# Optimization experiments

Measured on AMD Instinct MI355X. Metric: run time of the kernel, lower is better.

## Reference

```python
import jax, jax.numpy as jnp
import numpy as np

N_NODES = 50000
N_EDGES = 800000
NODE_F = 256
EDGE_F = 8
OUT_F = 64
NEG_SLOPE = 0.2
EPS = 1e-9


def _xavier(key, shape):
    # xavier_normal_ with gain=calculate_gain('relu')=sqrt(2)
    fan_out, fan_in = shape
    std = np.sqrt(2.0) * np.sqrt(2.0 / (fan_in + fan_out))
    return jax.random.normal(key, shape, dtype=jnp.float32) * std


def setup_inputs() -> dict:
    key = jax.random.key(0)
    ks = jax.random.split(key, 12)
    feat_src = jax.random.normal(ks[0], (N_NODES, NODE_F), dtype=jnp.float32)
    feat_edge = jax.random.normal(ks[1], (N_EDGES, EDGE_F), dtype=jnp.float32)
    src_idx = jax.random.randint(ks[2], (N_EDGES,), 0, N_NODES, dtype=jnp.int32)
    dst_idx = jax.random.randint(ks[3], (N_EDGES,), 0, N_NODES, dtype=jnp.int32)
    return {
        "feat_src": feat_src,
        "feat_edge": feat_edge,
        "src_idx": src_idx,
        "dst_idx": dst_idx,
        "W_src": _xavier(ks[4], (OUT_F, NODE_F)),
        "W_dst": _xavier(ks[5], (OUT_F, NODE_F)),
        "b_dst": jnp.zeros((OUT_F,), dtype=jnp.float32),
        "W_attn_src": _xavier(ks[6], (OUT_F, NODE_F)),
        "W_attn_dst": _xavier(ks[7], (OUT_F, NODE_F)),
        "W_attn_edge": _xavier(ks[8], (OUT_F, EDGE_F)),
        "scale": jnp.ones((1, OUT_F), dtype=jnp.float32),
        "offset": jnp.zeros((1, OUT_F), dtype=jnp.float32),
        "W_agg": _xavier(ks[9], (OUT_F, OUT_F)),
        "b_agg": jnp.zeros((OUT_F,), dtype=jnp.float32),
    }


def _edge_softmax(e, seg_idx, n_nodes):
    # per-segment (per-node) softmax over incident edges, channel-wise. e: [E, F]
    m = jax.ops.segment_max(e, seg_idx, num_segments=n_nodes)  # [N, F]
    m = jnp.where(jnp.isfinite(m), m, 0.0)  # empty segments -> safe value
    ex = jnp.exp(e - m[seg_idx])
    s = jax.ops.segment_sum(ex, seg_idx, num_segments=n_nodes)  # [N, F]
    return ex / s[seg_idx]


def reference(feat_src, feat_edge, src_idx, dst_idx,
              W_src, W_dst, b_dst, W_attn_src, W_attn_dst, W_attn_edge,
              scale, offset, W_agg, b_agg):
    n_nodes = feat_src.shape[0]
    feat_dst = feat_src  # graph is not a block

    # node/edge linear projections
    feat_src_fc = feat_src @ W_src.T                      # [N, F]
    attn_src = feat_src @ W_attn_src.T                    # [N, F]
    attn_dst = feat_dst @ W_attn_dst.T                    # [N, F]
    attn_edge = feat_edge @ W_attn_edge.T                 # [E, F]

    # u_add_v + u_add_e attention logits, then leaky_relu
    e = attn_src[src_idx] + attn_dst[dst_idx] + attn_edge  # [E, F]
    e = jax.nn.leaky_relu(e, NEG_SLOPE)

    # dual edge softmax (dst- and src-normalized), combined by sqrt-product
    a_dst = jnp.clip(_edge_softmax(e, dst_idx, n_nodes), EPS, None)
    a_src = jnp.clip(_edge_softmax(e, src_idx, n_nodes), EPS, None)
    a = jnp.sqrt(a_dst * a_src)                           # [E, F]

    # u_mul_e message + sum aggregation to destination nodes
    msg_sum = jax.ops.segment_sum(feat_src_fc[src_idx] * a, dst_idx,
                                  num_segments=n_nodes)   # [N, F]

    # agg_function: feature-dim norm (mean/var over last dim), then linear
    mean = jnp.mean(msg_sum, axis=-1, keepdims=True)
    var = jnp.var(msg_sum, axis=-1, keepdims=True) + EPS
    h = (msg_sum - mean) * scale * jax.lax.rsqrt(var) + offset
    rst = h @ W_agg.T + b_agg

    # residual dst projection (with bias)
    rst = rst + (feat_dst @ W_dst.T + b_dst)
    return rst
```

## Files before the change

kernel.cpp:

```cpp
#include <hip/hip_runtime.h>

#define N_NODES 50000
#define N_EDGES 800000
#define NODE_F 256
#define EDGE_F 8
#define OUT_F 64
#define M_PAD 50048
#define GEMM_BLOCKS 782
#define EDGE_BLOCKS 3125
#define FEAT_BLOCKS 6250

typedef unsigned int u32;
typedef unsigned short u16;
typedef __attribute__((ext_vector_type(8))) short bf16x8;
typedef __attribute__((ext_vector_type(4))) float f32x4;
typedef __attribute__((ext_vector_type(2))) _Float16 h2;

__device__ __forceinline__ u16 bf16r(float x) {
    u32 b = __float_as_uint(x);
    b += 0x7fffu + ((b >> 16) & 1u);
    return (u16)(b >> 16);
}
__device__ __forceinline__ u32 pk2(float a, float b) {
    return (u32)bf16r(a) | ((u32)bf16r(b) << 16);
}
__device__ __forceinline__ float bl(u32 u) { return __uint_as_float(u << 16); }
__device__ __forceinline__ float bh(u32 u) { return __uint_as_float(u & 0xffff0000u); }

__device__ __forceinline__ u32 pkh2(float a, float b) {
    union { h2 h; u32 u; } cv;
    cv.h[0] = (_Float16)a; cv.h[1] = (_Float16)b;
    return cv.u;
}
__device__ __forceinline__ h2 uh2(u32 u) {
    union { u32 u; h2 h; } cv; cv.u = u; return cv.h;
}
__device__ __forceinline__ float ae_dot(uint4 f, h2 w0, h2 w1, h2 w2, h2 w3) {
#if __has_builtin(__builtin_amdgcn_fdot2)
    float r = __builtin_amdgcn_fdot2(uh2(f.x), w0, 0.f, false);
    r = __builtin_amdgcn_fdot2(uh2(f.y), w1, r, false);
    r = __builtin_amdgcn_fdot2(uh2(f.z), w2, r, false);
    r = __builtin_amdgcn_fdot2(uh2(f.w), w3, r, false);
    return r;
#else
    h2 a0 = uh2(f.x), a1 = uh2(f.y), a2 = uh2(f.z), a3 = uh2(f.w);
    return (float)a0[0]*(float)w0[0] + (float)a0[1]*(float)w0[1]
         + (float)a1[0]*(float)w1[0] + (float)a1[1]*(float)w1[1]
         + (float)a2[0]*(float)w2[0] + (float)a2[1]*(float)w2[1]
         + (float)a3[0]*(float)w3[0] + (float)a3[1]*(float)w3[1];
#endif
}
#define LOAD_WH(c)                                                         \
    h2 wh0, wh1, wh2, wh3;                                                 \
    {                                                                      \
        float4 wa = *(const float4*)&W_ae[(c) * EDGE_F];                   \
        float4 wb = *(const float4*)&W_ae[(c) * EDGE_F + 4];               \
        wh0[0] = (_Float16)wa.x; wh0[1] = (_Float16)wa.y;                  \
        wh1[0] = (_Float16)wa.z; wh1[1] = (_Float16)wa.w;                  \
        wh2[0] = (_Float16)wb.x; wh2[1] = (_Float16)wb.y;                  \
        wh3[0] = (_Float16)wb.z; wh3[1] = (_Float16)wb.w;                  \
    }

__global__ __launch_bounds__(256) void hist_convert(
    const int* __restrict__ src_idx, const int* __restrict__ dst_idx,
    const float* __restrict__ feat,
    const float* __restrict__ W_src, const float* __restrict__ W_attn_src,
    const float* __restrict__ W_attn_dst, const float* __restrict__ W_dst,
    int* __restrict__ hist_src, int* __restrict__ hist_dst,
    u16* __restrict__ feat_bf, u16* __restrict__ Wb)
{
    int b = blockIdx.x;
    if (b < FEAT_BLOCKS) {
        size_t o = ((size_t)b * 256 + threadIdx.x) * 8;
        float4 v0 = *(const float4*)&feat[o];
        float4 v1 = *(const float4*)&feat[o + 4];
        uint4 p;
        p.x = pk2(v0.x, v0.y);
        p.y = pk2(v0.z, v0.w);
        p.z = pk2(v1.x, v1.y);
        p.w = pk2(v1.z, v1.w);
        *(uint4*)&feat_bf[o] = p;
    } else if (b < FEAT_BLOCKS + 256) {
        int t = (b - FEAT_BLOCKS) * 256 + threadIdx.x;
        int n = t >> 8, k = t & 255;
        int mat = n >> 6, oo = n & 63;
        const float* __restrict__ Ws[4] = {W_src, W_attn_src, W_attn_dst, W_dst};
        Wb[t] = bf16r(Ws[mat][oo * NODE_F + k]);
    } else {
        int e = (b - FEAT_BLOCKS - 256) * 256 + threadIdx.x;
        if (e >= N_EDGES) return;
        atomicAdd(&hist_src[src_idx[e]], 1);
        atomicAdd(&hist_dst[dst_idx[e]], 1);
    }
}

__global__ __launch_bounds__(512) void scan_kernel(
    const int* __restrict__ hist_dst, const int* __restrict__ hist_src,
    int* __restrict__ off_dst, int* __restrict__ off_src,
    int* __restrict__ cur_dst, int* __restrict__ cur_src)
{
    const int* __restrict__ h = blockIdx.x ? hist_src : hist_dst;
    int* __restrict__ off = blockIdx.x ? off_src : off_dst;
    int* __restrict__ cur = blockIdx.x ? cur_src : cur_dst;

    __shared__ int part[512];
    const int t = threadIdx.x;
    const int CH = (N_NODES + 511) / 512;
    int lo = t * CH, hi = min(lo + CH, N_NODES);
    int sum = 0;
    for (int i = lo; i < hi; ++i) sum += h[i];
    part[t] = sum;
    __syncthreads();
    for (int ofs = 1; ofs < 512; ofs <<= 1) {
        int v = (t >= ofs) ? part[t - ofs] : 0;
        __syncthreads();
        part[t] += v;
        __syncthreads();
    }
    int run = (t == 0) ? 0 : part[t - 1];
    for (int i = lo; i < hi; ++i) {
        off[i] = run;
        cur[i] = run;
        run += h[i];
    }
    if (t == 511) off[N_NODES] = run;
}

__global__ __launch_bounds__(256) void gemm_scatter(
    const u16* __restrict__ feat_bf, const u16* __restrict__ Wb,
    const float* __restrict__ b_dst,
    float* __restrict__ fc, u32* __restrict__ pack,
    u16* __restrict__ adst_bf, float* __restrict__ res,
    const int* __restrict__ src_idx, const int* __restrict__ dst_idx,
    const float* __restrict__ feat_edge,
    int* __restrict__ cur_src, int* __restrict__ cur_dst,
    int* __restrict__ adj_dst, int* __restrict__ adj_src,
    uint4* __restrict__ fh_src, uint4* __restrict__ fh_dst)
{
    if (blockIdx.x < GEMM_BLOCKS) {
        const int lane = threadIdx.x & 63;
        const int w = threadIdx.x >> 6;
        const int m0 = blockIdx.x * 64;
        const int lrow = lane & 15;
        const int lk = (lane >> 4) * 8;

        f32x4 acc[4][4] = {};
        const u16* Abase = feat_bf + (size_t)(m0 + lrow) * NODE_F + lk;
        const u16* Bbase = Wb + (size_t)(w * 64 + lrow) * NODE_F + lk;

#pragma unroll 2
        for (int ks = 0; ks < 8; ++ks) {
            const int k0 = ks * 32;
            bf16x8 a[4], bb[4];
#pragma unroll
            for (int r = 0; r < 4; ++r)
                a[r] = *(const bf16x8*)(Abase + (size_t)r * 16 * NODE_F + k0);
#pragma unroll
            for (int n = 0; n < 4; ++n)
                bb[n] = *(const bf16x8*)(Bbase + (size_t)n * 16 * NODE_F + k0);
#pragma unroll
            for (int r = 0; r < 4; ++r)
#pragma unroll
                for (int n = 0; n < 4; ++n)
                    acc[r][n] = __builtin_amdgcn_mfma_f32_16x16x32_bf16(
                        a[r], bb[n], acc[r][n], 0, 0, 0);
        }

        const int crow0 = (lane >> 4) * 4;
        const int ccol = lane & 15;
#pragma unroll
        for (int r = 0; r < 4; ++r) {
#pragma unroll
            for (int n = 0; n < 4; ++n) {
                const int col = n * 16 + ccol;
                const float bias = b_dst[col];
#pragma unroll
                for (int j = 0; j < 4; ++j) {
                    int row = m0 + r * 16 + crow0 + j;
                    if (row >= N_NODES) continue;
                    float v = acc[r][n][j];
                    size_t o = (size_t)row * 64 + col;
                    if (w == 0)      fc[o] = v;
                    else if (w == 1) pack[o] = (u32)bf16r(v);
                    else if (w == 2) adst_bf[o] = bf16r(v);
                    else             res[o] = v + bias;
                }
            }
        }
    } else {
        int e = (blockIdx.x - GEMM_BLOCKS) * 256 + threadIdx.x;
        if (e >= N_EDGES) return;
        int s = src_idx[e], d = dst_idx[e];
        float4 a0 = *(const float4*)&feat_edge[(size_t)e * EDGE_F];
        float4 a1 = *(const float4*)&feat_edge[(size_t)e * EDGE_F + 4];
        uint4 fv;
        fv.x = pkh2(a0.x, a0.y);
        fv.y = pkh2(a0.z, a0.w);
        fv.z = pkh2(a1.x, a1.y);
        fv.w = pkh2(a1.z, a1.w);
        int ps = atomicAdd(&cur_src[s], 1);
        adj_dst[ps] = d;
        fh_src[ps] = fv;
        int pd = atomicAdd(&cur_dst[d], 1);
        adj_src[pd] = s;
        fh_dst[pd] = fv;
    }
}

__global__ __launch_bounds__(256) void src_pass(
    const int* __restrict__ off_src, const int* __restrict__ adj_dst,
    const uint4* __restrict__ fh_src, const float* __restrict__ W_ae,
    u32* __restrict__ pack, const u16* __restrict__ adst_bf,
    const float* __restrict__ fc)
{
    int n = blockIdx.x * 4 + (threadIdx.x >> 6);
    int c = threadIdx.x & 63;

    LOAD_WH(c);
    u32 uown = pack[(size_t)n * 64 + c];
    float ac = bl(uown);

    int beg = __builtin_amdgcn_readfirstlane(off_src[n]);
    int end = __builtin_amdgcn_readfirstlane(off_src[n + 1]);
    float ssum = 0.f;
    int i = beg;
    for (; i + 3 < end; i += 4) {
        int d0 = adj_dst[i], d1 = adj_dst[i+1], d2 = adj_dst[i+2], d3 = adj_dst[i+3];
        uint4 f0 = fh_src[i], f1 = fh_src[i+1], f2 = fh_src[i+2], f3 = fh_src[i+3];
        float ad0 = __uint_as_float((u32)adst_bf[(size_t)d0 * 64 + c] << 16);
        float ad1 = __uint_as_float((u32)adst_bf[(size_t)d1 * 64 + c] << 16);
        float ad2 = __uint_as_float((u32)adst_bf[(size_t)d2 * 64 + c] << 16);
        float ad3 = __uint_as_float((u32)adst_bf[(size_t)d3 * 64 + c] << 16);
        float e0 = ac + ad0 + ae_dot(f0, wh0, wh1, wh2, wh3);
        float e1 = ac + ad1 + ae_dot(f1, wh0, wh1, wh2, wh3);
        float e2 = ac + ad2 + ae_dot(f2, wh0, wh1, wh2, wh3);
        float e3 = ac + ad3 + ae_dot(f3, wh0, wh1, wh2, wh3);
        e0 = fmaxf(e0, 0.2f * e0);
        e1 = fmaxf(e1, 0.2f * e1);
        e2 = fmaxf(e2, 0.2f * e2);
        e3 = fmaxf(e3, 0.2f * e3);
        ssum += __expf(e0) + __expf(e1) + __expf(e2) + __expf(e3);
    }
    for (; i < end; ++i) {
        int d0 = adj_dst[i];
        uint4 f0 = fh_src[i];
        float ad0 = __uint_as_float((u32)adst_bf[(size_t)d0 * 64 + c] << 16);
        float e0 = ac + ad0 + ae_dot(f0, wh0, wh1, wh2, wh3);
        e0 = fmaxf(e0, 0.2f * e0);
        ssum += __expf(e0);
    }
    float g = (ssum > 0.f) ? fc[(size_t)n * 64 + c] * rsqrtf(ssum) : 0.f;
    pack[(size_t)n * 64 + c] = (uown & 0xffffu) | ((u32)bf16r(g) << 16);
}

__global__ __launch_bounds__(256) void dst_fused_pass(
    const int* __restrict__ off_dst, const int* __restrict__ adj_src,
    const uint4* __restrict__ fh_dst, const float* __restrict__ W_ae,
    const u32* __restrict__ pack, const u16* __restrict__ adst_bf,
    const float* __restrict__ scale, const float* __restrict__ offset,
    const float* __restrict__ W_agg, const float* __restrict__ b_agg,
    const float* __restrict__ res, float* __restrict__ out)
{
    __shared__ float hbuf[4][OUT_F];
    int n = blockIdx.x * 4 + (threadIdx.x >> 6);
    int c = threadIdx.x & 63;
    int ln = threadIdx.x >> 6;

    LOAD_WH(c);
    float adc = __uint_as_float((u32)adst_bf[(size_t)n * 64 + c] << 16);

    int beg = __builtin_amdgcn_readfirstlane(off_dst[n]);
    int end = __builtin_amdgcn_readfirstlane(off_dst[n + 1]);
    float sd = 0.f, mm = 0.f;
    int i = beg;
    for (; i + 3 < end; i += 4) {
        int s0 = adj_src[i], s1 = adj_src[i+1], s2 = adj_src[i+2], s3 = adj_src[i+3];
        uint4 f0 = fh_dst[i], f1 = fh_dst[i+1], f2 = fh_dst[i+2], f3 = fh_dst[i+3];
        u32 u0 = pack[(size_t)s0 * 64 + c];
        u32 u1 = pack[(size_t)s1 * 64 + c];
        u32 u2 = pack[(size_t)s2 * 64 + c];
        u32 u3 = pack[(size_t)s3 * 64 + c];
        float e0 = bl(u0) + adc + ae_dot(f0, wh0, wh1, wh2, wh3);
        float e1 = bl(u1) + adc + ae_dot(f1, wh0, wh1, wh2, wh3);
        float e2 = bl(u2) + adc + ae_dot(f2, wh0, wh1, wh2, wh3);
        float e3 = bl(u3) + adc + ae_dot(f3, wh0, wh1, wh2, wh3);
        e0 = fmaxf(e0, 0.2f * e0);
        e1 = fmaxf(e1, 0.2f * e1);
        e2 = fmaxf(e2, 0.2f * e2);
        e3 = fmaxf(e3, 0.2f * e3);
        float ex0 = __expf(e0), ex1 = __expf(e1), ex2 = __expf(e2), ex3 = __expf(e3);
        sd += ex0 + ex1 + ex2 + ex3;
        mm += ex0 * bh(u0) + ex1 * bh(u1) + ex2 * bh(u2) + ex3 * bh(u3);
    }
    for (; i < end; ++i) {
        int s0 = adj_src[i];
        uint4 f0 = fh_dst[i];
        u32 u0 = pack[(size_t)s0 * 64 + c];
        float e0 = bl(u0) + adc + ae_dot(f0, wh0, wh1, wh2, wh3);
        e0 = fmaxf(e0, 0.2f * e0);
        float ex0 = __expf(e0);
        sd += ex0;
        mm += ex0 * bh(u0);
    }
    float x = (sd > 0.f) ? mm * rsqrtf(sd) : 0.f;

    float s1 = x, s2 = x * x;
#pragma unroll
    for (int off = 32; off; off >>= 1) {
        s1 += __shfl_xor(s1, off, 64);
        s2 += __shfl_xor(s2, off, 64);
    }
    float mean = s1 * (1.f / OUT_F);
    float var = fmaxf(s2 * (1.f / OUT_F) - mean * mean, 0.f) + 1e-9f;
    float h = (x - mean) * scale[c] * rsqrtf(var) + offset[c];
    hbuf[ln][c] = h;

    float acc = 0.f;
#pragma unroll
    for (int j = 0; j < OUT_F; j += 4) {
        float4 w = *(const float4*)&W_agg[c * OUT_F + j];
        acc += w.x * hbuf[ln][j] + w.y * hbuf[ln][j + 1]
             + w.z * hbuf[ln][j + 2] + w.w * hbuf[ln][j + 3];
    }
    out[(size_t)n * OUT_F + c] = acc + b_agg[c] + res[(size_t)n * OUT_F + c];
}

extern "C" void kernel_launch(void* const* d_in, const int* in_sizes, int n_in,
                              void* d_out, int out_size, void* d_ws, size_t ws_size,
                              hipStream_t stream) {
    const float* feat_src    = (const float*)d_in[0];
    const float* feat_edge   = (const float*)d_in[1];
    const int*   src_idx     = (const int*)d_in[2];
    const int*   dst_idx     = (const int*)d_in[3];
    const float* W_src       = (const float*)d_in[4];
    const float* W_dst       = (const float*)d_in[5];
    const float* b_dst       = (const float*)d_in[6];
    const float* W_attn_src  = (const float*)d_in[7];
    const float* W_attn_dst  = (const float*)d_in[8];
    const float* W_attn_edge = (const float*)d_in[9];
    const float* scale       = (const float*)d_in[10];
    const float* offset      = (const float*)d_in[11];
    const float* W_agg       = (const float*)d_in[12];
    const float* b_agg       = (const float*)d_in[13];
    float* out = (float*)d_out;

    const size_t NF = (size_t)N_NODES * OUT_F;

    char* base = (char*)d_ws;
    float* fc      = (float*)base;                 base += NF * 4;
    float* res     = (float*)base;                 base += NF * 4;
    u32*   pack    = (u32*)base;                   base += NF * 4;
    u16*   feat_bf = (u16*)base;                   base += (size_t)M_PAD * NODE_F * 2;
    u16*   Wb      = (u16*)base;                   base += 256 * 256 * 2;
    uint4* fh_src  = (uint4*)base;                 base += (size_t)N_EDGES * 16;
    uint4* fh_dst  = (uint4*)base;                 base += (size_t)N_EDGES * 16;
    u16*   adst_bf = (u16*)base;                   base += NF * 2;
    int*   hist_dst = (int*)base;                  base += N_NODES * 4;
    int*   hist_src = (int*)base;                  base += N_NODES * 4;
    int*   off_dst  = (int*)base;                  base += (N_NODES + 1) * 4;
    int*   off_src  = (int*)base;                  base += (N_NODES + 1) * 4;
    int*   cur_dst  = (int*)base;                  base += N_NODES * 4;
    int*   cur_src  = (int*)base;                  base += N_NODES * 4;
    int*   adj_dst  = (int*)base;                  base += (size_t)N_EDGES * 4;
    int*   adj_src  = (int*)base;                  base += (size_t)N_EDGES * 4;

    hipMemsetAsync(hist_dst, 0, 2 * N_NODES * sizeof(int), stream);

    hist_convert<<<FEAT_BLOCKS + 256 + EDGE_BLOCKS, 256, 0, stream>>>(
        src_idx, dst_idx, feat_src, W_src, W_attn_src, W_attn_dst, W_dst,
        hist_src, hist_dst, feat_bf, Wb);

    scan_kernel<<<2, 512, 0, stream>>>(hist_dst, hist_src, off_dst, off_src,
                                       cur_dst, cur_src);

    gemm_scatter<<<GEMM_BLOCKS + EDGE_BLOCKS, 256, 0, stream>>>(
        feat_bf, Wb, b_dst, fc, pack, adst_bf, res,
        src_idx, dst_idx, feat_edge, cur_src, cur_dst,
        adj_dst, adj_src, fh_src, fh_dst);

    const int nb = N_NODES / 4;
    src_pass<<<nb, 256, 0, stream>>>(off_src, adj_dst, fh_src, W_attn_edge,
                                     pack, adst_bf, fc);
    dst_fused_pass<<<nb, 256, 0, stream>>>(off_dst, adj_src, fh_dst, W_attn_edge,
                                           pack, adst_bf, scale, offset,
                                           W_agg, b_agg, res, out);
}
```

Baseline: 451.7 us.

## Fuse feature bf16 conversion into GEMM and interleave adjacency entries

Drops the separate pass that converted the node features to bf16. The GEMM now loads fp32 rows directly and packs them to bf16 by truncation with a byte permute, with row indices clamped in place of padding. The separate adjacency-index and edge-feature arrays are merged into one 32-byte entry struct, so each edge's neighbor index and fp16 features share a cache line in the gather passes. The trade-offs are twice the bytes per GEMM A load, truncation in place of round-to-nearest, and padding bytes in each entry.

```diff
diff --git a/kernel.cpp b/kernel.cpp
--- a/kernel.cpp
+++ b/kernel.cpp
@@ -8,7 +8,6 @@
 #define M_PAD 50048
 #define GEMM_BLOCKS 782
 #define EDGE_BLOCKS 3125
-#define FEAT_BLOCKS 6250
 
 typedef unsigned int u32;
 typedef unsigned short u16;
@@ -16,16 +15,28 @@
 typedef __attribute__((ext_vector_type(4))) float f32x4;
 typedef __attribute__((ext_vector_type(2))) _Float16 h2;
 
+struct __align__(32) Ent { int opp; int p0; int p1; int p2; uint4 fh; };
+
 __device__ __forceinline__ u16 bf16r(float x) {
     u32 b = __float_as_uint(x);
     b += 0x7fffu + ((b >> 16) & 1u);
     return (u16)(b >> 16);
 }
-__device__ __forceinline__ u32 pk2(float a, float b) {
-    return (u32)bf16r(a) | ((u32)bf16r(b) << 16);
-}
 __device__ __forceinline__ float bl(u32 u) { return __uint_as_float(u << 16); }
 __device__ __forceinline__ float bh(u32 u) { return __uint_as_float(u & 0xffff0000u); }
+
+__device__ __forceinline__ u32 pktr(float lo, float hi) {
+    return __builtin_amdgcn_perm(__float_as_uint(hi), __float_as_uint(lo),
+                                 0x07060302);
+}
+__device__ __forceinline__ bf16x8 pack_bf8(float4 a, float4 b) {
+    union { bf16x8 v; u32 u[4]; } r;
+    r.u[0] = pktr(a.x, a.y);
+    r.u[1] = pktr(a.z, a.w);
+    r.u[2] = pktr(b.x, b.y);
+    r.u[3] = pktr(b.z, b.w);
+    return r.v;
+}
 
 __device__ __forceinline__ u32 pkh2(float a, float b) {
     union { h2 h; u32 u; } cv;
@@ -61,33 +72,22 @@
         wh3[0] = (_Float16)wb.z; wh3[1] = (_Float16)wb.w;                  \
     }
 
-__global__ __launch_bounds__(256) void hist_convert(
+__global__ __launch_bounds__(256) void setup_kernel(
     const int* __restrict__ src_idx, const int* __restrict__ dst_idx,
-    const float* __restrict__ feat,
     const float* __restrict__ W_src, const float* __restrict__ W_attn_src,
     const float* __restrict__ W_attn_dst, const float* __restrict__ W_dst,
     int* __restrict__ hist_src, int* __restrict__ hist_dst,
-    u16* __restrict__ feat_bf, u16* __restrict__ Wb)
+    u16* __restrict__ Wb)
 {
     int b = blockIdx.x;
-    if (b < FEAT_BLOCKS) {
-        size_t o = ((size_t)b * 256 + threadIdx.x) * 8;
-        float4 v0 = *(const float4*)&feat[o];
-        float4 v1 = *(const float4*)&feat[o + 4];
-        uint4 p;
-        p.x = pk2(v0.x, v0.y);
-        p.y = pk2(v0.z, v0.w);
-        p.z = pk2(v1.x, v1.y);
-        p.w = pk2(v1.z, v1.w);
-        *(uint4*)&feat_bf[o] = p;
-    } else if (b < FEAT_BLOCKS + 256) {
-        int t = (b - FEAT_BLOCKS) * 256 + threadIdx.x;
+    if (b < 256) {
+        int t = b * 256 + threadIdx.x;
         int n = t >> 8, k = t & 255;
         int mat = n >> 6, oo = n & 63;
         const float* __restrict__ Ws[4] = {W_src, W_attn_src, W_attn_dst, W_dst};
         Wb[t] = bf16r(Ws[mat][oo * NODE_F + k]);
     } else {
-        int e = (b - FEAT_BLOCKS - 256) * 256 + threadIdx.x;
+        int e = (b - 256) * 256 + threadIdx.x;
         if (e >= N_EDGES) return;
         atomicAdd(&hist_src[src_idx[e]], 1);
         atomicAdd(&hist_dst[dst_idx[e]], 1);
@@ -127,15 +127,14 @@
 }
 
 __global__ __launch_bounds__(256) void gemm_scatter(
-    const u16* __restrict__ feat_bf, const u16* __restrict__ Wb,
+    const float* __restrict__ feat, const u16* __restrict__ Wb,
     const float* __restrict__ b_dst,
     float* __restrict__ fc, u32* __restrict__ pack,
     u16* __restrict__ adst_bf, float* __restrict__ res,
     const int* __restrict__ src_idx, const int* __restrict__ dst_idx,
     const float* __restrict__ feat_edge,
     int* __restrict__ cur_src, int* __restrict__ cur_dst,
-    int* __restrict__ adj_dst, int* __restrict__ adj_src,
-    uint4* __restrict__ fh_src, uint4* __restrict__ fh_dst)
+    Ent* __restrict__ ent_src, Ent* __restrict__ ent_dst)
 {
     if (blockIdx.x < GEMM_BLOCKS) {
         const int lane = threadIdx.x & 63;
@@ -144,17 +143,26 @@
         const int lrow = lane & 15;
         const int lk = (lane >> 4) * 8;
 
+        const float* Arow[4];
+#pragma unroll
+        for (int r = 0; r < 4; ++r) {
+            int rr = min(m0 + r * 16 + lrow, N_NODES - 1);
+            Arow[r] = feat + (size_t)rr * NODE_F + lk;
+        }
+        const u16* Bbase = Wb + (size_t)(w * 64 + lrow) * NODE_F + lk;
+
         f32x4 acc[4][4] = {};
-        const u16* Abase = feat_bf + (size_t)(m0 + lrow) * NODE_F + lk;
-        const u16* Bbase = Wb + (size_t)(w * 64 + lrow) * NODE_F + lk;
 
 #pragma unroll 2
         for (int ks = 0; ks < 8; ++ks) {
             const int k0 = ks * 32;
             bf16x8 a[4], bb[4];
 #pragma unroll
-            for (int r = 0; r < 4; ++r)
-                a[r] = *(const bf16x8*)(Abase + (size_t)r * 16 * NODE_F + k0);
+            for (int r = 0; r < 4; ++r) {
+                float4 a0 = *(const float4*)(Arow[r] + k0);
+                float4 a1 = *(const float4*)(Arow[r] + k0 + 4);
+                a[r] = pack_bf8(a0, a1);
+            }
 #pragma unroll
             for (int n = 0; n < 4; ++n)
                 bb[n] = *(const bf16x8*)(Bbase + (size_t)n * 16 * NODE_F + k0);
@@ -199,17 +207,17 @@
         fv.z = pkh2(a1.x, a1.y);
         fv.w = pkh2(a1.z, a1.w);
         int ps = atomicAdd(&cur_src[s], 1);
-        adj_dst[ps] = d;
-        fh_src[ps] = fv;
+        ent_src[ps].opp = d;
+        ent_src[ps].fh = fv;
         int pd = atomicAdd(&cur_dst[d], 1);
-        adj_src[pd] = s;
-        fh_dst[pd] = fv;
+        ent_dst[pd].opp = s;
+        ent_dst[pd].fh = fv;
     }
 }
 
 __global__ __launch_bounds__(256) void src_pass(
-    const int* __restrict__ off_src, const int* __restrict__ adj_dst,
-    const uint4* __restrict__ fh_src, const float* __restrict__ W_ae,
+    const int* __restrict__ off_src, const Ent* __restrict__ ent,
+    const float* __restrict__ W_ae,
     u32* __restrict__ pack, const u16* __restrict__ adst_bf,
     const float* __restrict__ fc)
 {
@@ -225,8 +233,8 @@
     float ssum = 0.f;
     int i = beg;
     for (; i + 3 < end; i += 4) {
-        int d0 = adj_dst[i], d1 = adj_dst[i+1], d2 = adj_dst[i+2], d3 = adj_dst[i+3];
-        uint4 f0 = fh_src[i], f1 = fh_src[i+1], f2 = fh_src[i+2], f3 = fh_src[i+3];
+        int d0 = ent[i].opp, d1 = ent[i+1].opp, d2 = ent[i+2].opp, d3 = ent[i+3].opp;
+        uint4 f0 = ent[i].fh, f1 = ent[i+1].fh, f2 = ent[i+2].fh, f3 = ent[i+3].fh;
         float ad0 = __uint_as_float((u32)adst_bf[(size_t)d0 * 64 + c] << 16);
         float ad1 = __uint_as_float((u32)adst_bf[(size_t)d1 * 64 + c] << 16);
         float ad2 = __uint_as_float((u32)adst_bf[(size_t)d2 * 64 + c] << 16);
@@ -242,8 +250,8 @@
         ssum += __expf(e0) + __expf(e1) + __expf(e2) + __expf(e3);
     }
     for (; i < end; ++i) {
-        int d0 = adj_dst[i];
-        uint4 f0 = fh_src[i];
+        int d0 = ent[i].opp;
+        uint4 f0 = ent[i].fh;
         float ad0 = __uint_as_float((u32)adst_bf[(size_t)d0 * 64 + c] << 16);
         float e0 = ac + ad0 + ae_dot(f0, wh0, wh1, wh2, wh3);
         e0 = fmaxf(e0, 0.2f * e0);
@@ -254,8 +262,8 @@
 }
 
 __global__ __launch_bounds__(256) void dst_fused_pass(
-    const int* __restrict__ off_dst, const int* __restrict__ adj_src,
-    const uint4* __restrict__ fh_dst, const float* __restrict__ W_ae,
+    const int* __restrict__ off_dst, const Ent* __restrict__ ent,
+    const float* __restrict__ W_ae,
     const u32* __restrict__ pack, const u16* __restrict__ adst_bf,
     const float* __restrict__ scale, const float* __restrict__ offset,
     const float* __restrict__ W_agg, const float* __restrict__ b_agg,
@@ -274,8 +282,8 @@
     float sd = 0.f, mm = 0.f;
     int i = beg;
     for (; i + 3 < end; i += 4) {
-        int s0 = adj_src[i], s1 = adj_src[i+1], s2 = adj_src[i+2], s3 = adj_src[i+3];
-        uint4 f0 = fh_dst[i], f1 = fh_dst[i+1], f2 = fh_dst[i+2], f3 = fh_dst[i+3];
+        int s0 = ent[i].opp, s1 = ent[i+1].opp, s2 = ent[i+2].opp, s3 = ent[i+3].opp;
+        uint4 f0 = ent[i].fh, f1 = ent[i+1].fh, f2 = ent[i+2].fh, f3 = ent[i+3].fh;
         u32 u0 = pack[(size_t)s0 * 64 + c];
         u32 u1 = pack[(size_t)s1 * 64 + c];
         u32 u2 = pack[(size_t)s2 * 64 + c];
@@ -293,8 +301,8 @@
         mm += ex0 * bh(u0) + ex1 * bh(u1) + ex2 * bh(u2) + ex3 * bh(u3);
     }
     for (; i < end; ++i) {
-        int s0 = adj_src[i];
-        uint4 f0 = fh_dst[i];
+        int s0 = ent[i].opp;
+        uint4 f0 = ent[i].fh;
         u32 u0 = pack[(size_t)s0 * 64 + c];
         float e0 = bl(u0) + adc + ae_dot(f0, wh0, wh1, wh2, wh3);
         e0 = fmaxf(e0, 0.2f * e0);
@@ -350,38 +358,35 @@
     float* fc      = (float*)base;                 base += NF * 4;
     float* res     = (float*)base;                 base += NF * 4;
     u32*   pack    = (u32*)base;                   base += NF * 4;
-    u16*   feat_bf = (u16*)base;                   base += (size_t)M_PAD * NODE_F * 2;
     u16*   Wb      = (u16*)base;                   base += 256 * 256 * 2;
-    uint4* fh_src  = (uint4*)base;                 base += (size_t)N_EDGES * 16;
-    uint4* fh_dst  = (uint4*)base;                 base += (size_t)N_EDGES * 16;
     u16*   adst_bf = (u16*)base;                   base += NF * 2;
+    Ent*   ent_src = (Ent*)base;                   base += (size_t)N_EDGES * 32;
+    Ent*   ent_dst = (Ent*)base;                   base += (size_t)N_EDGES * 32;
     int*   hist_dst = (int*)base;                  base += N_NODES * 4;
     int*   hist_src = (int*)base;                  base += N_NODES * 4;
     int*   off_dst  = (int*)base;                  base += (N_NODES + 1) * 4;
     int*   off_src  = (int*)base;                  base += (N_NODES + 1) * 4;
     int*   cur_dst  = (int*)base;                  base += N_NODES * 4;
     int*   cur_src  = (int*)base;                  base += N_NODES * 4;
-    int*   adj_dst  = (int*)base;                  base += (size_t)N_EDGES * 4;
-    int*   adj_src  = (int*)base;                  base += (size_t)N_EDGES * 4;
 
     hipMemsetAsync(hist_dst, 0, 2 * N_NODES * sizeof(int), stream);
 
-    hist_convert<<<FEAT_BLOCKS + 256 + EDGE_BLOCKS, 256, 0, stream>>>(
-        src_idx, dst_idx, feat_src, W_src, W_attn_src, W_attn_dst, W_dst,
-        hist_src, hist_dst, feat_bf, Wb);
+    setup_kernel<<<256 + EDGE_BLOCKS, 256, 0, stream>>>(
+        src_idx, dst_idx, W_src, W_attn_src, W_attn_dst, W_dst,
+        hist_src, hist_dst, Wb);
 
     scan_kernel<<<2, 512, 0, stream>>>(hist_dst, hist_src, off_dst, off_src,
                                        cur_dst, cur_src);
 
     gemm_scatter<<<GEMM_BLOCKS + EDGE_BLOCKS, 256, 0, stream>>>(
-        feat_bf, Wb, b_dst, fc, pack, adst_bf, res,
+        feat_src, Wb, b_dst, fc, pack, adst_bf, res,
         src_idx, dst_idx, feat_edge, cur_src, cur_dst,
-        adj_dst, adj_src, fh_src, fh_dst);
+        ent_src, ent_dst);
 
     const int nb = N_NODES / 4;
-    src_pass<<<nb, 256, 0, stream>>>(off_src, adj_dst, fh_src, W_attn_edge,
+    src_pass<<<nb, 256, 0, stream>>>(off_src, ent_src, W_attn_edge,
                                      pack, adst_bf, fc);
-    dst_fused_pass<<<nb, 256, 0, stream>>>(off_dst, adj_src, fh_dst, W_attn_edge,
+    dst_fused_pass<<<nb, 256, 0, stream>>>(off_dst, ent_dst, W_attn_edge,
                                            pack, adst_bf, scale, offset,
                                            W_agg, b_agg, res, out);
 }
```

New measurement: 453.5 us. About the same (+0.4%).
